# Kernel optimization log

Hardware: AMD Instinct MI355X
Metric: run time of the kernel (lower is better)

## Reference

```python
import jax, jax.numpy as jnp
import numpy as np

N_NODES = 20000
N_EDGES = 100000
NODE_IN = 16
EDGE_IN = 10
LEAK = 0.1
EPS = 1e-5


def setup_inputs() -> dict:
    key = jax.random.key(0)
    ks = iter(jax.random.split(key, 40))

    def rn(shape, scale):
        return jax.random.normal(next(ks), shape, dtype=jnp.float32) * scale

    inp = {}
    inp["x"] = jax.random.normal(next(ks), (N_NODES, NODE_IN), dtype=jnp.float32)
    inp["e"] = jax.random.normal(next(ks), (N_EDGES, EDGE_IN), dtype=jnp.float32)
    inp["edge_index"] = jax.random.randint(next(ks), (2, N_EDGES), 0, N_NODES, dtype=jnp.int64)
    inp["xbatch"] = jnp.zeros((N_NODES,), dtype=jnp.int64)

    # BatchNorm affine params
    inp["bn_node_g"] = jnp.ones((NODE_IN,), jnp.float32)
    inp["bn_node_b"] = jnp.zeros((NODE_IN,), jnp.float32)
    inp["bn_edge_g"] = jnp.ones((EDGE_IN,), jnp.float32)
    inp["bn_edge_b"] = jnp.zeros((EDGE_IN,), jnp.float32)

    # nn1: Lin(10,16) -> LeakyReLU -> Lin(16, 16*32) -> LeakyReLU
    inp["nn1_w1"] = rn((EDGE_IN, 16), 0.3); inp["nn1_b1"] = jnp.zeros((16,), jnp.float32)
    inp["nn1_w2"] = rn((16, 16 * 32), 0.25); inp["nn1_b2"] = jnp.zeros((16 * 32,), jnp.float32)
    # nn2: Lin(10,32) -> LeakyReLU -> Lin(32, 32*64) -> LeakyReLU
    inp["nn2_w1"] = rn((EDGE_IN, 32), 0.3); inp["nn2_b1"] = jnp.zeros((32,), jnp.float32)
    inp["nn2_w2"] = rn((32, 32 * 64), 0.18); inp["nn2_b2"] = jnp.zeros((32 * 64,), jnp.float32)

    # NNConv root weights + biases
    inp["l1_root"] = rn((16, 32), 0.25); inp["l1_bias"] = jnp.zeros((32,), jnp.float32)
    inp["l2_root"] = rn((32, 64), 0.18); inp["l2_bias"] = jnp.zeros((64,), jnp.float32)

    # edge_pred_mlp: 138 -> 64 -> 32 -> 16 -> 8 -> 2
    dims = [2 * 64 + EDGE_IN, 64, 32, 16, 8, 2]
    for i in range(5):
        inp[f"mlp_w{i+1}"] = rn((dims[i], dims[i + 1]), 1.0 / np.sqrt(dims[i]))
        inp[f"mlp_b{i+1}"] = jnp.zeros((dims[i + 1],), jnp.float32)
    return inp


def _bn(v, g, b):
    # BatchNorm1d, training-mode batch statistics (biased variance), eps=1e-5
    m = v.mean(axis=0)
    var = v.var(axis=0)
    return (v - m) * jax.lax.rsqrt(var + EPS) * g + b


def _lrelu(v):
    return jax.nn.leaky_relu(v, LEAK)


def _nnconv(x, src, dst, e, w1, b1, w2, b2, root, bias, c_in, c_out):
    # edge MLP -> per-edge weight matrix [E, c_in, c_out]
    h = _lrelu(e @ w1 + b1)
    W = _lrelu(h @ w2 + b2).reshape(-1, c_in, c_out)
    # gather source features, per-edge matmul, scatter-add to targets
    msg = jnp.einsum("ei,eio->eo", x[src], W)
    agg = jax.ops.segment_sum(msg, dst, num_segments=x.shape[0])
    return agg + x @ root + bias


def reference(x, e, edge_index, xbatch,
              bn_node_g, bn_node_b, bn_edge_g, bn_edge_b,
              nn1_w1, nn1_b1, nn1_w2, nn1_b2,
              nn2_w1, nn2_b1, nn2_w2, nn2_b2,
              l1_root, l1_bias, l2_root, l2_bias,
              mlp_w1, mlp_b1, mlp_w2, mlp_b2, mlp_w3, mlp_b3,
              mlp_w4, mlp_b4, mlp_w5, mlp_b5):
    src, dst = edge_index[0], edge_index[1]
    e = _bn(e, bn_edge_g, bn_edge_b)
    x = _bn(x, bn_node_g, bn_node_b)
    x = _nnconv(x, src, dst, e, nn1_w1, nn1_b1, nn1_w2, nn1_b2, l1_root, l1_bias, 16, 32)
    x = _nnconv(x, src, dst, e, nn2_w1, nn2_b1, nn2_w2, nn2_b2, l2_root, l2_bias, 32, 64)
    # MetaLayer edge model: cat(source, target, edge_attr) -> MLP -> [E, 2]
    h = jnp.concatenate([x[src], x[dst], e], axis=1)
    h = _lrelu(h @ mlp_w1 + mlp_b1)
    h = _lrelu(h @ mlp_w2 + mlp_b2)
    h = _lrelu(h @ mlp_w3 + mlp_b3)
    h = _lrelu(h @ mlp_w4 + mlp_b4)
    edge_pred = h @ mlp_w5 + mlp_b5
    return edge_pred
```

## Files before the change

kernel.cpp:

```cpp
#include <hip/hip_runtime.h>
#include <cstdint>

#define N_NODES 20000
#define N_EDGES 100000
#define BN_EPS 1e-5f
#define SCAN_BLKS 79

typedef __attribute__((ext_vector_type(8))) short short8;
typedef __attribute__((ext_vector_type(4))) float floatx4;
typedef __attribute__((ext_vector_type(2))) float float2v;

__device__ __forceinline__ float lrelu(float v) { return fmaxf(v, 0.1f * v); }
__device__ __forceinline__ float4 ld4(const float* p) { return *reinterpret_cast<const float4*>(p); }
__device__ __forceinline__ float2 ld2(const float* p) { return *reinterpret_cast<const float2*>(p); }

__device__ __forceinline__ void atomAddF(float* p, float v) {
#if defined(__HIP_DEVICE_COMPILE__)
    unsafeAtomicAdd(p, v);
#else
    atomicAdd(p, v);
#endif
}

__device__ __forceinline__ unsigned short f2bf(float f) {
    union { float f; uint32_t u; } v; v.f = f;
    uint32_t r = v.u + 0x7fffu + ((v.u >> 16) & 1u);
    return (unsigned short)(r >> 16);
}
__device__ __forceinline__ uint32_t pack2(float a, float b) {
    return (uint32_t)f2bf(a) | ((uint32_t)f2bf(b) << 16);
}
__device__ __forceinline__ short8 pack8(float4 a, float4 b) {
    union { short8 s; uint32_t u[4]; } r;
    r.u[0] = pack2(a.x, a.y); r.u[1] = pack2(a.z, a.w);
    r.u[2] = pack2(b.x, b.y); r.u[3] = pack2(b.z, b.w);
    return r.s;
}

__device__ void stats10_dev(const float* __restrict__ v, int rows, float* __restrict__ out,
                            int blk, int nblk, float* sh) {
    if (threadIdx.x < 20) sh[threadIdx.x] = 0.f;
    __syncthreads();
    int nf2 = rows * 5;
    int stride = nblk * 256;
    int g = blk * 256 + threadIdx.x;
    int c2 = g % 5;
    float s0 = 0.f, s1 = 0.f, q0 = 0.f, q1 = 0.f;
    const float2* p = reinterpret_cast<const float2*>(v);
    for (int i = g; i < nf2; i += stride) {
        float2 t = p[i];
        s0 += t.x; s1 += t.y; q0 += t.x * t.x; q1 += t.y * t.y;
    }
    atomicAdd(&sh[2 * c2], s0);
    atomicAdd(&sh[2 * c2 + 1], s1);
    atomicAdd(&sh[10 + 2 * c2], q0);
    atomicAdd(&sh[10 + 2 * c2 + 1], q1);
    __syncthreads();
    if (threadIdx.x < 20) atomAddF(&out[threadIdx.x], sh[threadIdx.x]);
}

__device__ void stats16_dev(const float* __restrict__ v, int rows, float* __restrict__ out,
                            int blk, int nblk, float* sh) {
    if (threadIdx.x < 32) sh[threadIdx.x] = 0.f;
    __syncthreads();
    int nf4 = rows * 4;
    int stride = nblk * 256;
    int g = blk * 256 + threadIdx.x;
    int cg = (g & 3) * 4;
    float s[4] = {0.f, 0.f, 0.f, 0.f}, q[4] = {0.f, 0.f, 0.f, 0.f};
    const float4* p = reinterpret_cast<const float4*>(v);
    for (int i = g; i < nf4; i += stride) {
        float4 t = p[i];
        s[0] += t.x; s[1] += t.y; s[2] += t.z; s[3] += t.w;
        q[0] += t.x * t.x; q[1] += t.y * t.y; q[2] += t.z * t.z; q[3] += t.w * t.w;
    }
    #pragma unroll
    for (int off = 32; off >= 4; off >>= 1) {
        #pragma unroll
        for (int j = 0; j < 4; ++j) {
            s[j] += __shfl_down(s[j], off, 64);
            q[j] += __shfl_down(q[j], off, 64);
        }
    }
    if ((threadIdx.x & 63) < 4) {
        #pragma unroll
        for (int j = 0; j < 4; ++j) {
            atomicAdd(&sh[cg + j], s[j]);
            atomicAdd(&sh[16 + cg + j], q[j]);
        }
    }
    __syncthreads();
    if (threadIdx.x < 32) atomAddF(&out[threadIdx.x], sh[threadIdx.x]);
}

template<int CIN, int COUT, int H, int OCH>
__device__ void convpack_row(const float* __restrict__ w2, const float* __restrict__ b2,
                             char* __restrict__ pk, int r) {
    constexpr int NROW = CIN * OCH;
    constexpr int WB = NROW * 64;
    constexpr int PACKB = WB + NROW * 4;
    if (r >= CIN * COUT) return;
    int chunk = r / NROW;
    int rem = r % NROW;
    int i = rem / OCH, ol = rem % OCH;
    int n = i * COUT + chunk * OCH + ol;
    char* base = pk + (size_t)chunk * PACKB;
    uint32_t pkv[16];
    #pragma unroll
    for (int t = 0; t < 16; ++t) pkv[t] = 0;
    #pragma unroll
    for (int k = 0; k < H; k += 2)
        pkv[k >> 1] = pack2(w2[(size_t)k * (CIN * COUT) + n],
                            w2[(size_t)(k + 1) * (CIN * COUT) + n]);
    uint4* ob = reinterpret_cast<uint4*>(base);
    #pragma unroll
    for (int q = 0; q < 4; ++q)
        ob[(size_t)q * NROW + rem] = make_uint4(pkv[4 * q], pkv[4 * q + 1],
                                                pkv[4 * q + 2], pkv[4 * q + 3]);
    ((float*)(base + WB))[rem] = b2[n];
}

#define P1_S10 120
#define P1_S16 120
__global__ __launch_bounds__(256)
void prep1_kernel(const float* __restrict__ e, const float* __restrict__ x,
                  float* __restrict__ stats_e, float* __restrict__ stats_x,
                  const int* __restrict__ dst, int* __restrict__ counts,
                  const float* __restrict__ nn1_w2, const float* __restrict__ nn1_b2, char* __restrict__ cpack1,
                  const float* __restrict__ nn2_w2, const float* __restrict__ nn2_b2, char* __restrict__ cpack2,
                  const float* __restrict__ mw1, unsigned short* __restrict__ w1t,
                  const float* __restrict__ mw2, const float* __restrict__ mb2,
                  const float* __restrict__ mw3, const float* __restrict__ mb3,
                  const float* __restrict__ mw4, const float* __restrict__ mb4,
                  const float* __restrict__ mw5, const float* __restrict__ mb5,
                  float* __restrict__ mlpw)
{
    __shared__ float sh[32];
    int b = blockIdx.x;
    if (b < P1_S10) {
        stats10_dev(e, N_EDGES, stats_e, b, P1_S10, sh);
    } else if (b < P1_S10 + P1_S16) {
        stats16_dev(x, N_NODES, stats_x, b - P1_S10, P1_S16, sh);
    } else if (b < 631) {
        int i = (b - 240) * 256 + threadIdx.x;
        if (i < N_EDGES) atomicAdd(&counts[dst[i]], 1);
    } else if (b < 633) {
        convpack_row<16, 32, 16, 32>(nn1_w2, nn1_b2, cpack1, (b - 631) * 256 + threadIdx.x);
    } else if (b < 641) {
        convpack_row<32, 64, 32, 16>(nn2_w2, nn2_b2, cpack2, (b - 633) * 256 + threadIdx.x);
    } else {
        if (threadIdx.x < 64) {
            int o = threadIdx.x;
            for (int k = 0; k < 160; k += 2) {
                float a = (k < 138) ? mw1[(size_t)k * 64 + o] : 0.f;
                float c = (k + 1 < 138) ? mw1[(size_t)(k + 1) * 64 + o] : 0.f;
                *reinterpret_cast<uint32_t*>(w1t + (size_t)o * 160 + k) = pack2(a, c);
            }
        }
        for (int i = threadIdx.x; i < 2764; i += 256) {
            float v = 0.f;
            if (i < 2048) v = mw2[i];
            else if (i < 2560) v = mw3[i - 2048];
            else if (i < 2688) v = mw4[i - 2560];
            else if (i < 2704) v = mw5[i - 2688];
            else if (i < 2736) v = mb2[i - 2704];
            else if (i < 2752) v = mb3[i - 2736];
            else if (i < 2760) v = mb4[i - 2752];
            else if (i < 2762) v = mb5[i - 2760];
            mlpw[i] = v;
        }
    }
}

__global__ __launch_bounds__(256)
void scanA_kernel(const int* __restrict__ counts, int* __restrict__ bsum, int n) {
    __shared__ int sh[4];
    int b = blockIdx.x, t = threadIdx.x;
    int i = b * 256 + t;
    int v = (i < n) ? counts[i] : 0;
    #pragma unroll
    for (int off = 32; off > 0; off >>= 1) v += __shfl_down(v, off, 64);
    if ((t & 63) == 0) sh[t >> 6] = v;
    __syncthreads();
    if (t == 0) bsum[b] = sh[0] + sh[1] + sh[2] + sh[3];
}

__global__ __launch_bounds__(256)
void scanC_kernel(const int* __restrict__ counts, const int* __restrict__ bsum,
                  int* __restrict__ starts, int* __restrict__ cursor, int n) {
    __shared__ int ws[4];
    __shared__ int bs[SCAN_BLKS];
    int b = blockIdx.x, t = threadIdx.x;
    if (t < SCAN_BLKS) bs[t] = bsum[t];
    int i = b * 256 + t;
    int val = (i < n) ? counts[i] : 0;
    int lane = t & 63, wv = t >> 6;
    int v = val;
    #pragma unroll
    for (int off = 1; off < 64; off <<= 1) {
        int u = __shfl_up(v, off, 64);
        if (lane >= off) v += u;
    }
    if (lane == 63) ws[wv] = v;
    __syncthreads();
    int woff = 0;
    for (int w = 0; w < wv; ++w) woff += ws[w];
    int boff = 0;
    for (int w = 0; w < b; ++w) boff += bs[w];
    int ex = boff + woff + v - val;
    if (i < n) { starts[i] = ex; cursor[i] = ex; }
}

#define P2_N16 1250
#define P2_SCAT 391
#define P2_HGEN 782
__global__ __launch_bounds__(256)
void prep2_kernel(const float* __restrict__ x, const float* __restrict__ stats_x,
                  const float* __restrict__ bn_node_g, const float* __restrict__ bn_node_b,
                  float* __restrict__ x_n,
                  const int* __restrict__ dst, int* __restrict__ cursor, int* __restrict__ epos,
                  const float* __restrict__ e, const float* __restrict__ stats_e,
                  const float* __restrict__ bn_edge_g, const float* __restrict__ bn_edge_b,
                  float* __restrict__ e_n,
                  const float* __restrict__ w1a, const float* __restrict__ b1a,
                  const float* __restrict__ w1b, const float* __restrict__ b1b,
                  unsigned short* __restrict__ h1, unsigned short* __restrict__ h2)
{
    int b = blockIdx.x;
    if (b < P2_N16) {
        int idx = b * 256 + threadIdx.x;
        if (idx >= N_NODES * 16) return;
        int c = idx & 15;
        float N = (float)N_NODES;
        float m = stats_x[c] / N;
        float var = stats_x[16 + c] / N - m * m;
        float sc = rsqrtf(var + BN_EPS) * bn_node_g[c];
        x_n[idx] = (x[idx] - m) * sc + bn_node_b[c];
    } else if (b < P2_N16 + P2_SCAT) {
        int i = (b - P2_N16) * 256 + threadIdx.x;
        if (i < N_EDGES) {
            int p = atomicAdd(&cursor[dst[i]], 1);
            epos[i] = p;
        }
    } else {
        int g = (b - P2_N16 - P2_SCAT) * 256 + threadIdx.x;
        if (g >= 2 * N_EDGES) return;
        int eg = g >> 1, hh = g & 1;
        float ev[10];
        float Ecnt = (float)N_EDGES;
        #pragma unroll
        for (int j = 0; j < 10; ++j) {
            float m = stats_e[j] / Ecnt;
            float var = stats_e[10 + j] / Ecnt - m * m;
            float sc = rsqrtf(var + BN_EPS) * bn_edge_g[j];
            ev[j] = (e[(size_t)eg * 10 + j] - m) * sc + bn_edge_b[j];
        }
        if (hh == 0) {
            #pragma unroll
            for (int j = 0; j < 10; ++j) e_n[(size_t)eg * 10 + j] = ev[j];
        }
        {
            uint32_t pk[4];
            #pragma unroll
            for (int pp = 0; pp < 4; ++pp) {
                int k = (hh * 4 + pp) * 2;
                float a0 = b1a[k], a1 = b1a[k + 1];
                #pragma unroll
                for (int j = 0; j < 10; ++j) {
                    a0 += ev[j] * w1a[j * 16 + k];
                    a1 += ev[j] * w1a[j * 16 + k + 1];
                }
                pk[pp] = pack2(lrelu(a0), lrelu(a1));
            }
            uint4* o = reinterpret_cast<uint4*>(h1 + (size_t)eg * 32);
            o[hh] = make_uint4(pk[0], pk[1], pk[2], pk[3]);
            o[2 + hh] = make_uint4(0, 0, 0, 0);
        }
        {
            uint32_t pk[8];
            #pragma unroll
            for (int pp = 0; pp < 8; ++pp) {
                int k = (hh * 8 + pp) * 2;
                float a0 = b1b[k], a1 = b1b[k + 1];
                #pragma unroll
                for (int j = 0; j < 10; ++j) {
                    a0 += ev[j] * w1b[j * 32 + k];
                    a1 += ev[j] * w1b[j * 32 + k + 1];
                }
                pk[pp] = pack2(lrelu(a0), lrelu(a1));
            }
            uint4* o = reinterpret_cast<uint4*>(h2 + (size_t)eg * 32);
            o[hh * 2]     = make_uint4(pk[0], pk[1], pk[2], pk[3]);
            o[hh * 2 + 1] = make_uint4(pk[4], pk[5], pk[6], pk[7]);
        }
    }
}

template<int CIN, int COUT, int OCH, int NE, int IB>
__global__ __launch_bounds__(512, 4)
void conv_lds_kernel(const unsigned short* __restrict__ hbuf,
                     const char* __restrict__ pack,
                     const int* __restrict__ src,
                     const int* __restrict__ epos,
                     const float* __restrict__ xin,
                     float* __restrict__ msgbuf,
                     int n_edges)
{
    constexpr int NCH = COUT / OCH;
    constexpr int NROW = CIN * OCH;
    constexpr int WB = NROW * 64;
    constexpr int PACKB = WB + NROW * 4;
    constexpr int NOT = OCH / 16;
    __shared__ char smem[PACKB];

    int tid = threadIdx.x;
    int chunk = blockIdx.x % NCH;
    int eblk = blockIdx.x / NCH;

    {
        const uint4* g = reinterpret_cast<const uint4*>(pack + (size_t)chunk * PACKB);
        uint4* s = reinterpret_cast<uint4*>(smem);
        #pragma unroll 1
        for (int o = tid; o < PACKB / 16; o += 512) s[o] = g[o];
    }
    __syncthreads();

    int wv = tid >> 6, lane = tid & 63;
    int el = lane & 15, quad = lane >> 4;
    int g0 = (eblk * 8 + wv) * NE;
    if (g0 * 16 >= n_edges) return;

    const unsigned short* wlds = reinterpret_cast<const unsigned short*>(smem)
                                 + ((size_t)quad * NROW + el) * 8;
    const float* blds = reinterpret_cast<const float*>(smem + WB) + quad * 4;

    int sg[NE], slot[NE];
    short8 bfrag[NE];
    #pragma unroll
    for (int g = 0; g < NE; ++g) {
        int e0 = (g0 + g) * 16;
        int e = (e0 < n_edges) ? (e0 + el) : el;
        sg[g] = src[e];
        slot[g] = epos[e];
        bfrag[g] = *reinterpret_cast<const short8*>(hbuf + (size_t)e * 32 + quad * 8);
    }

    float2v msg0[NE][NOT], msg1[NE][NOT];
    #pragma unroll
    for (int g = 0; g < NE; ++g)
        #pragma unroll
        for (int t = 0; t < NOT; ++t) {
            msg0[g][t] = (float2v){0.f, 0.f};
            msg1[g][t] = (float2v){0.f, 0.f};
        }

    const float2v pt = {0.1f, 0.1f};

    #pragma unroll 1
    for (int ib = 0; ib < CIN / IB; ++ib) {
        float xs[NE][IB];
        #pragma unroll
        for (int g = 0; g < NE; ++g) {
            #pragma unroll
            for (int t = 0; t < IB; t += 4) {
                float4 v = ld4(xin + (size_t)sg[g] * CIN + ib * IB + t);
                xs[g][t] = v.x; xs[g][t + 1] = v.y; xs[g][t + 2] = v.z; xs[g][t + 3] = v.w;
            }
        }
        #pragma unroll
        for (int ii = 0; ii < IB; ++ii) {
            int i = ib * IB + ii;
            #pragma unroll
            for (int ot = 0; ot < NOT; ++ot) {
                short8 af = *reinterpret_cast<const short8*>(wlds + (i * OCH + ot * 16) * 8);
                float4 bb = *reinterpret_cast<const float4*>(blds + i * OCH + ot * 16);
                floatx4 cinit = {bb.x, bb.y, bb.z, bb.w};
                #pragma unroll
                for (int g = 0; g < NE; ++g) {
                    floatx4 c = __builtin_amdgcn_mfma_f32_16x16x32_bf16(af, bfrag[g], cinit, 0, 0, 0);
                    float2v c0 = {c[0], c[1]}, c1 = {c[2], c[3]};
                    float2v m0 = __builtin_elementwise_max(c0, c0 * pt);
                    float2v m1 = __builtin_elementwise_max(c1, c1 * pt);
                    float2v xi2 = {xs[g][ii], xs[g][ii]};
                    msg0[g][ot] += xi2 * m0;
                    msg1[g][ot] += xi2 * m1;
                }
            }
        }
    }

    #pragma unroll
    for (int g = 0; g < NE; ++g) {
        if ((g0 + g) * 16 >= n_edges) break;
        float* orow = msgbuf + (size_t)slot[g] * COUT + chunk * OCH;
        #pragma unroll
        for (int ot = 0; ot < NOT; ++ot)
            *reinterpret_cast<float4*>(orow + ot * 16 + quad * 4) =
                make_float4(msg0[g][ot][0], msg0[g][ot][1], msg1[g][ot][0], msg1[g][ot][1]);
    }
}

template<int CIN, int C>
__global__ __launch_bounds__(256)
void gather_root_kernel(const float* __restrict__ xin, const float* __restrict__ w,
                        const float* __restrict__ bias,
                        const float* __restrict__ msg,
                        const int* __restrict__ starts, const int* __restrict__ counts,
                        float* __restrict__ xout, int nodes)
{
    constexpr int NPW = 64 / C;
    int wv = blockIdx.x * 4 + (threadIdx.x >> 6);
    int lane = threadIdx.x & 63;
    int node = wv * NPW + lane / C;
    int ch = lane % C;
    if (node >= nodes) return;
    float acc = bias[ch];
    const float* xrow = xin + (size_t)node * CIN;
    #pragma unroll
    for (int i = 0; i < CIN; ++i) acc += xrow[i] * w[i * C + ch];
    int s0 = starts[node], cnt = counts[node];
    const float* mrow = msg + (size_t)s0 * C + ch;
    int i = 0;
    for (; i + 3 < cnt; i += 4) {
        float m0 = mrow[(size_t)(i)     * C];
        float m1 = mrow[(size_t)(i + 1) * C];
        float m2 = mrow[(size_t)(i + 2) * C];
        float m3 = mrow[(size_t)(i + 3) * C];
        acc += (m0 + m1) + (m2 + m3);
    }
    for (; i < cnt; ++i) acc += mrow[(size_t)i * C];
    xout[(size_t)node * C + ch] = acc;
}

__global__ __launch_bounds__(256)
void mlp2_kernel(const float* __restrict__ x2, const float* __restrict__ e_n,
                 const int* __restrict__ src, const int* __restrict__ dst,
                 const unsigned short* __restrict__ w1t, const float* __restrict__ b1,
                 const float* __restrict__ mlpw,
                 float* __restrict__ out, int n_edges)
{
    __shared__ float wl[2764];
    __shared__ float a1t[4 * 1092];
    __shared__ float a2scr[4 * 528];

    int tid = threadIdx.x;
    {
        const uint4* g = reinterpret_cast<const uint4*>(mlpw);
        uint4* s = reinterpret_cast<uint4*>(wl);
        #pragma unroll 1
        for (int i = tid; i < 691; i += 256) s[i] = g[i];
    }

    int wv = tid >> 6, lane = tid & 63;
    int el = lane & 15, quad = lane >> 4;
    int e = blockIdx.x * 64 + wv * 16 + el;
    int eS = (e < n_edges) ? e : (n_edges - 1);
    int sN = src[eS], dN = dst[eS];

    short8 bf[5];
    {
        const float* rs = x2 + (size_t)sN * 64 + quad * 8;
        const float* rd = x2 + (size_t)dN * 64 + quad * 8;
        bf[0] = pack8(ld4(rs), ld4(rs + 4));
        bf[1] = pack8(ld4(rs + 32), ld4(rs + 36));
        bf[2] = pack8(ld4(rd), ld4(rd + 4));
        bf[3] = pack8(ld4(rd + 32), ld4(rd + 36));
        union { short8 s; uint32_t u[4]; } t;
        t.u[0] = t.u[1] = t.u[2] = t.u[3] = 0;
        const float* ep = e_n + (size_t)eS * 10;
        if (quad == 0) {
            float2 p0 = ld2(ep), p1 = ld2(ep + 2), p2 = ld2(ep + 4), p3 = ld2(ep + 6);
            t.u[0] = pack2(p0.x, p0.y); t.u[1] = pack2(p1.x, p1.y);
            t.u[2] = pack2(p2.x, p2.y); t.u[3] = pack2(p3.x, p3.y);
        } else if (quad == 1) {
            float2 p4 = ld2(ep + 8);
            t.u[0] = pack2(p4.x, p4.y);
        }
        bf[4] = t.s;
    }

    float* slab = &a1t[wv * 1092];
    {
        floatx4 acc[4];
        #pragma unroll
        for (int ot = 0; ot < 4; ++ot) {
            float4 bb = ld4(b1 + ot * 16 + quad * 4);
            acc[ot] = (floatx4){bb.x, bb.y, bb.z, bb.w};
        }
        #pragma unroll
        for (int ks = 0; ks < 5; ++ks) {
            #pragma unroll
            for (int ot = 0; ot < 4; ++ot) {
                short8 af = *reinterpret_cast<const short8*>(
                    w1t + (size_t)(ot * 16 + el) * 160 + ks * 32 + quad * 8);
                acc[ot] = __builtin_amdgcn_mfma_f32_16x16x32_bf16(af, bf[ks], acc[ot], 0, 0, 0);
            }
        }
        #pragma unroll
        for (int ot = 0; ot < 4; ++ot) {
            #pragma unroll
            for (int r = 0; r < 4; ++r)
                slab[(ot * 16 + quad * 4 + r) * 17 + el] = lrelu(acc[ot][r]);
        }
    }
    __syncthreads();

    const float* w2l = wl;            const float* w3l = wl + 2048;
    const float* w4l = wl + 2560;     const float* w5l = wl + 2688;
    const float* b2l = wl + 2704;     const float* b3l = wl + 2736;
    const float* b4l = wl + 2752;     const float* b5l = wl + 2760;
    float* a2s = &a2scr[wv * 528];
    float* a3s = slab;
    float* a4s = slab + 512;
    int p = quad;

    {
        float a2[8];
        #pragma unroll
        for (int j = 0; j < 8; ++j) a2[j] = b2l[p * 8 + j];
        #pragma unroll 4
        for (int i = 0; i < 64; ++i) {
            float ai = slab[i * 17 + el];
            #pragma unroll
            for (int j = 0; j < 8; ++j) a2[j] += ai * w2l[i * 32 + p * 8 + j];
        }
        #pragma unroll
        for (int j = 0; j < 8; ++j) a2s[el * 33 + p * 8 + j] = lrelu(a2[j]);
    }
    {
        float a3[4];
        #pragma unroll
        for (int j = 0; j < 4; ++j) a3[j] = b3l[p * 4 + j];
        #pragma unroll 4
        for (int i = 0; i < 32; ++i) {
            float ai = a2s[el * 33 + i];
            #pragma unroll
            for (int j = 0; j < 4; ++j) a3[j] += ai * w3l[i * 16 + p * 4 + j];
        }
        #pragma unroll
        for (int j = 0; j < 4; ++j) a3s[el * 17 + p * 4 + j] = lrelu(a3[j]);
    }
    {
        float a4[2];
        a4[0] = b4l[p * 2]; a4[1] = b4l[p * 2 + 1];
        #pragma unroll
        for (int i = 0; i < 16; ++i) {
            float ai = a3s[el * 17 + i];
            a4[0] += ai * w4l[i * 8 + p * 2];
            a4[1] += ai * w4l[i * 8 + p * 2 + 1];
        }
        a4s[el * 9 + p * 2]     = lrelu(a4[0]);
        a4s[el * 9 + p * 2 + 1] = lrelu(a4[1]);
    }
    if (p < 2) {
        float o = b5l[p];
        #pragma unroll
        for (int i = 0; i < 8; ++i) o += a4s[el * 9 + i] * w5l[i * 2 + p];
        if (e < n_edges) out[(size_t)e * 2 + p] = o;
    }
}

extern "C" void kernel_launch(void* const* d_in, const int* in_sizes, int n_in,
                              void* d_out, int out_size, void* d_ws, size_t ws_size,
                              hipStream_t stream)
{
    const float* x  = (const float*)d_in[0];
    const float* e  = (const float*)d_in[1];
    const int*   ei = (const int*)d_in[2];
    const float* bn_node_g = (const float*)d_in[4];
    const float* bn_node_b = (const float*)d_in[5];
    const float* bn_edge_g = (const float*)d_in[6];
    const float* bn_edge_b = (const float*)d_in[7];
    const float* nn1_w1 = (const float*)d_in[8];
    const float* nn1_b1 = (const float*)d_in[9];
    const float* nn1_w2 = (const float*)d_in[10];
    const float* nn1_b2 = (const float*)d_in[11];
    const float* nn2_w1 = (const float*)d_in[12];
    const float* nn2_b1 = (const float*)d_in[13];
    const float* nn2_w2 = (const float*)d_in[14];
    const float* nn2_b2 = (const float*)d_in[15];
    const float* l1_root = (const float*)d_in[16];
    const float* l1_bias = (const float*)d_in[17];
    const float* l2_root = (const float*)d_in[18];
    const float* l2_bias = (const float*)d_in[19];
    const float* mw1 = (const float*)d_in[20]; const float* mb1 = (const float*)d_in[21];
    const float* mw2 = (const float*)d_in[22]; const float* mb2 = (const float*)d_in[23];
    const float* mw3 = (const float*)d_in[24]; const float* mb3 = (const float*)d_in[25];
    const float* mw4 = (const float*)d_in[26]; const float* mb4 = (const float*)d_in[27];
    const float* mw5 = (const float*)d_in[28]; const float* mb5 = (const float*)d_in[29];

    const int* src = ei;
    const int* dst = ei + N_EDGES;

    float* ws = (float*)d_ws;
    float* stats_e = ws;
    float* stats_x = ws + 32;
    int* counts = (int*)(ws + 64);
    int* starts = counts + 20000;
    int* cursor = starts + 20000;
    int* epos   = cursor + 20000;
    int* bsum   = epos + 100000;
    float* e_n = ws + 64 + 160128;
    float* x_n = e_n + 1000000;
    float* x1  = x_n + 320000;
    float* x2  = x1 + 640000;
    float* msg = x2 + 1280000;
    unsigned short* h1   = (unsigned short*)(msg + 6400000);
    unsigned short* h2   = h1 + 3200000;
    unsigned short* w1t  = h2 + 3200000;
    char* cpack1 = (char*)(w1t + 10240);
    char* cpack2 = cpack1 + 34816;
    float* mlpw = (float*)(cpack2 + 4 * 34816);
    float* out = (float*)d_out;

    (void)hipMemsetAsync(d_ws, 0, (64 + 20000) * 4, stream);

    prep1_kernel<<<642, 256, 0, stream>>>(
        e, x, stats_e, stats_x, dst, counts,
        nn1_w2, nn1_b2, cpack1, nn2_w2, nn2_b2, cpack2,
        mw1, w1t, mw2, mb2, mw3, mb3, mw4, mb4, mw5, mb5, mlpw);

    scanA_kernel<<<SCAN_BLKS, 256, 0, stream>>>(counts, bsum, N_NODES);
    scanC_kernel<<<SCAN_BLKS, 256, 0, stream>>>(counts, bsum, starts, cursor, N_NODES);

    prep2_kernel<<<P2_N16 + P2_SCAT + P2_HGEN, 256, 0, stream>>>(
        x, stats_x, bn_node_g, bn_node_b, x_n,
        dst, cursor, epos,
        e, stats_e, bn_edge_g, bn_edge_b, e_n,
        nn1_w1, nn1_b1, nn2_w1, nn2_b1, h1, h2);

    const int NGRP = (N_EDGES + 15) / 16;
    const int CB = (NGRP + 31) / 32;

    conv_lds_kernel<16, 32, 32, 4, 4><<<CB, 512, 0, stream>>>(h1, cpack1, src, epos, x_n, msg, N_EDGES);
    gather_root_kernel<16, 32><<<(N_NODES / 2 + 3) / 4, 256, 0, stream>>>(
        x_n, l1_root, l1_bias, msg, starts, counts, x1, N_NODES);

    conv_lds_kernel<32, 64, 16, 4, 8><<<CB * 4, 512, 0, stream>>>(h2, cpack2, src, epos, x1, msg, N_EDGES);
    gather_root_kernel<32, 64><<<(N_NODES + 3) / 4, 256, 0, stream>>>(
        x1, l2_root, l2_bias, msg, starts, counts, x2, N_NODES);

    mlp2_kernel<<<(N_EDGES + 63) / 64, 256, 0, stream>>>(
        x2, e_n, src, dst, w1t, mb1, mlpw, out, N_EDGES);
}
```

Before: 273.1 us.

## Widen layer-2 conv output chunk to 32 and read bias from global

For the second NNConv the packed weight chunk now covers 32 output channels instead of 16, so it is split into two chunks instead of four. Bias is no longer packed into LDS; it is read from the global nn2_b2 array. Each wave now handles 2 edge groups instead of 4, which changes the grid to keep the edge coverage. This cuts how often each edge's h fragment, x row and src/epos indices are reloaded across chunks, at the cost of more LDS per block and extra global bias loads inside the inner loop.

Result: slower. 282.9 us (+3.6%).

```diff
diff --git a/kernel.cpp b/kernel.cpp
--- a/kernel.cpp
+++ b/kernel.cpp
@@ -120,6 +120,30 @@
     ((float*)(base + WB))[rem] = b2[n];
 }
 
+template<int CIN, int COUT, int H, int OCH>
+__device__ void convpack2w_row(const float* __restrict__ w2, char* __restrict__ pk, int r) {
+    constexpr int NROW = CIN * OCH;
+    constexpr int WB = NROW * 64;
+    if (r >= CIN * COUT) return;
+    int chunk = r / NROW;
+    int rem = r % NROW;
+    int i = rem / OCH, ol = rem % OCH;
+    int n = i * COUT + chunk * OCH + ol;
+    char* base = pk + (size_t)chunk * WB;
+    uint32_t pkv[16];
+    #pragma unroll
+    for (int t = 0; t < 16; ++t) pkv[t] = 0;
+    #pragma unroll
+    for (int k = 0; k < H; k += 2)
+        pkv[k >> 1] = pack2(w2[(size_t)k * (CIN * COUT) + n],
+                            w2[(size_t)(k + 1) * (CIN * COUT) + n]);
+    uint4* ob = reinterpret_cast<uint4*>(base);
+    #pragma unroll
+    for (int q = 0; q < 4; ++q)
+        ob[(size_t)q * NROW + rem] = make_uint4(pkv[4 * q], pkv[4 * q + 1],
+                                                pkv[4 * q + 2], pkv[4 * q + 3]);
+}
+
 #define P1_S10 120
 #define P1_S16 120
 __global__ __launch_bounds__(256)
@@ -127,7 +151,7 @@
                   float* __restrict__ stats_e, float* __restrict__ stats_x,
                   const int* __restrict__ dst, int* __restrict__ counts,
                   const float* __restrict__ nn1_w2, const float* __restrict__ nn1_b2, char* __restrict__ cpack1,
-                  const float* __restrict__ nn2_w2, const float* __restrict__ nn2_b2, char* __restrict__ cpack2,
+                  const float* __restrict__ nn2_w2, char* __restrict__ cpack2,
                   const float* __restrict__ mw1, unsigned short* __restrict__ w1t,
                   const float* __restrict__ mw2, const float* __restrict__ mb2,
                   const float* __restrict__ mw3, const float* __restrict__ mb3,
@@ -147,7 +171,7 @@
     } else if (b < 633) {
         convpack_row<16, 32, 16, 32>(nn1_w2, nn1_b2, cpack1, (b - 631) * 256 + threadIdx.x);
     } else if (b < 641) {
-        convpack_row<32, 64, 32, 16>(nn2_w2, nn2_b2, cpack2, (b - 633) * 256 + threadIdx.x);
+        convpack2w_row<32, 64, 32, 32>(nn2_w2, cpack2, (b - 633) * 256 + threadIdx.x);
     } else {
         if (threadIdx.x < 64) {
             int o = threadIdx.x;
@@ -296,10 +320,11 @@
     }
 }
 
-template<int CIN, int COUT, int OCH, int NE, int IB>
-__global__ __launch_bounds__(512, 4)
+template<int CIN, int COUT, int OCH, int NE, int IB, bool GBIAS, int WAVES>
+__global__ __launch_bounds__(WAVES * 64, 4)
 void conv_lds_kernel(const unsigned short* __restrict__ hbuf,
                      const char* __restrict__ pack,
+                     const float* __restrict__ b2g,
                      const int* __restrict__ src,
                      const int* __restrict__ epos,
                      const float* __restrict__ xin,
@@ -309,7 +334,7 @@
     constexpr int NCH = COUT / OCH;
     constexpr int NROW = CIN * OCH;
     constexpr int WB = NROW * 64;
-    constexpr int PACKB = WB + NROW * 4;
+    constexpr int PACKB = GBIAS ? WB : (WB + NROW * 4);
     constexpr int NOT = OCH / 16;
     __shared__ char smem[PACKB];
 
@@ -321,18 +346,19 @@
         const uint4* g = reinterpret_cast<const uint4*>(pack + (size_t)chunk * PACKB);
         uint4* s = reinterpret_cast<uint4*>(smem);
         #pragma unroll 1
-        for (int o = tid; o < PACKB / 16; o += 512) s[o] = g[o];
+        for (int o = tid; o < PACKB / 16; o += WAVES * 64) s[o] = g[o];
     }
     __syncthreads();
 
     int wv = tid >> 6, lane = tid & 63;
     int el = lane & 15, quad = lane >> 4;
-    int g0 = (eblk * 8 + wv) * NE;
+    int g0 = (eblk * WAVES + wv) * NE;
     if (g0 * 16 >= n_edges) return;
 
     const unsigned short* wlds = reinterpret_cast<const unsigned short*>(smem)
                                  + ((size_t)quad * NROW + el) * 8;
-    const float* blds = reinterpret_cast<const float*>(smem + WB) + quad * 4;
+    const float* blds = GBIAS ? (b2g + chunk * OCH + quad * 4)
+                              : (reinterpret_cast<const float*>(smem + WB) + quad * 4);
 
     int sg[NE], slot[NE];
     short8 bfrag[NE];
@@ -373,7 +399,8 @@
             #pragma unroll
             for (int ot = 0; ot < NOT; ++ot) {
                 short8 af = *reinterpret_cast<const short8*>(wlds + (i * OCH + ot * 16) * 8);
-                float4 bb = *reinterpret_cast<const float4*>(blds + i * OCH + ot * 16);
+                float4 bb = GBIAS ? ld4(blds + i * COUT + ot * 16)
+                                  : *reinterpret_cast<const float4*>(blds + i * OCH + ot * 16);
                 floatx4 cinit = {bb.x, bb.y, bb.z, bb.w};
                 #pragma unroll
                 for (int g = 0; g < NE; ++g) {
@@ -610,14 +637,14 @@
     unsigned short* w1t  = h2 + 3200000;
     char* cpack1 = (char*)(w1t + 10240);
     char* cpack2 = cpack1 + 34816;
-    float* mlpw = (float*)(cpack2 + 4 * 34816);
+    float* mlpw = (float*)(cpack2 + 2 * 65536);
     float* out = (float*)d_out;
 
     (void)hipMemsetAsync(d_ws, 0, (64 + 20000) * 4, stream);
 
     prep1_kernel<<<642, 256, 0, stream>>>(
         e, x, stats_e, stats_x, dst, counts,
-        nn1_w2, nn1_b2, cpack1, nn2_w2, nn2_b2, cpack2,
+        nn1_w2, nn1_b2, cpack1, nn2_w2, cpack2,
         mw1, w1t, mw2, mb2, mw3, mb3, mw4, mb4, mw5, mb5, mlpw);
 
     scanA_kernel<<<SCAN_BLKS, 256, 0, stream>>>(counts, bsum, N_NODES);
@@ -630,13 +657,16 @@
         nn1_w1, nn1_b1, nn2_w1, nn2_b1, h1, h2);
 
     const int NGRP = (N_EDGES + 15) / 16;
-    const int CB = (NGRP + 31) / 32;
-
-    conv_lds_kernel<16, 32, 32, 4, 4><<<CB, 512, 0, stream>>>(h1, cpack1, src, epos, x_n, msg, N_EDGES);
+
+    const int CB1 = (NGRP + 31) / 32;
+    conv_lds_kernel<16, 32, 32, 4, 4, false, 8><<<CB1, 512, 0, stream>>>(
+        h1, cpack1, nullptr, src, epos, x_n, msg, N_EDGES);
     gather_root_kernel<16, 32><<<(N_NODES / 2 + 3) / 4, 256, 0, stream>>>(
         x_n, l1_root, l1_bias, msg, starts, counts, x1, N_NODES);
 
-    conv_lds_kernel<32, 64, 16, 4, 8><<<CB * 4, 512, 0, stream>>>(h2, cpack2, src, epos, x1, msg, N_EDGES);
+    const int CB2 = (NGRP + 15) / 16;
+    conv_lds_kernel<32, 64, 32, 2, 8, true, 8><<<CB2 * 2, 512, 0, stream>>>(
+        h2, cpack2, nn2_b2, src, epos, x1, msg, N_EDGES);
     gather_root_kernel<32, 64><<<(N_NODES + 3) / 4, 256, 0, stream>>>(
         x1, l2_root, l2_bias, msg, starts, counts, x2, N_NODES);
 
```
